# Kernel optimization log

Measured on AMD Instinct MI355X. Metric: run time of the kernel, lower is better.

Reference implementation:

```python
import jax, jax.numpy as jnp
import numpy as np

B = 512       # batch_size
IN = 256      # input_size
H = 512       # hidden_size
OUT = 64      # output_size
N_PAIRS = B - 1   # number of H0 persistence deaths (connected components merges)
TOL = 1e-6    # rtol for torch.isclose
ATOL = 1e-8   # torch default atol
EPS = 0.0     # homology_eps
TARGET_P = 1.0
HOM_P = 1.0
COMP_P = 0.01

_IU = np.triu_indices(B, 1)  # condensed pdist indexing, static


def _mlp(batch, W1, b1, W2, b2, W3, b3, Wout, bout):
    # FeedForward: input->hidden, (n_layers-1) hidden->hidden, hidden->output, ReLU
    h = jax.nn.relu(batch @ W1 + b1)
    h = jax.nn.relu(h @ W2 + b2)
    h = jax.nn.relu(h @ W3 + b3)
    return h @ Wout + bout


def _pdist(y):
    # condensed euclidean pairwise distances, same ordering as torch F.pdist
    d = y[_IU[0]] - y[_IU[1]]                 # [P, OUT]
    return jnp.sqrt(jnp.sum(d * d, axis=-1))  # [P]


def setup_inputs() -> dict:
    key = jax.random.key(0)
    ks = jax.random.split(key, 8)
    batch = jax.random.normal(ks[0], (B, IN), jnp.float32)
    target = jax.random.normal(ks[1], (B, OUT), jnp.float32)
    W1 = jax.random.normal(ks[2], (IN, H), jnp.float32) / np.sqrt(IN)
    W2 = jax.random.normal(ks[3], (H, H), jnp.float32) / np.sqrt(H)
    W3 = jax.random.normal(ks[4], (H, H), jnp.float32) / np.sqrt(H)
    Wout = jax.random.normal(ks[5], (H, OUT), jnp.float32) / np.sqrt(H)
    b1 = jnp.zeros((H,), jnp.float32)
    b2 = jnp.zeros((H,), jnp.float32)
    b3 = jnp.zeros((H,), jnp.float32)
    bout = jnp.zeros((OUT,), jnp.float32)
    # persistence deaths = actual critical pdist values (from the external
    # Vietoris-Rips routine in the original); sample N_PAIRS distinct entries.
    y0 = _mlp(batch, W1, b1, W2, b2, W3, b3, Wout, bout)
    pd0 = np.asarray(_pdist(y0))
    idx = np.random.default_rng(0).choice(pd0.shape[0], N_PAIRS, replace=False)
    persistence_deaths = jnp.asarray(pd0[idx], jnp.float32)
    return {"batch": batch, "target": target,
            "W1": W1, "b1": b1, "W2": W2, "b2": b2, "W3": W3, "b3": b3,
            "Wout": Wout, "bout": bout,
            "persistence_deaths": persistence_deaths}


def reference(batch, target, W1, b1, W2, b2, W3, b3, Wout, bout, persistence_deaths):
    y = _mlp(batch, W1, b1, W2, b2, W3, b3, Wout, bout)   # [B, OUT]
    y_hom = y  # normalize_for_homology = False
    pd = _pdist(y_hom)                                     # [P]
    # vectorized indicator_death over all pairs (replaces per-pair Python loop)
    mask = jnp.any(jnp.isclose(pd[:, None], persistence_deaths[None, :],
                               rtol=TOL, atol=ATOL), axis=1)      # [P] bool
    # homology_dim=0: birth_pdist = 0; norm=1 of selected (death - 0 + eps)
    homology_loss = jnp.sum(jnp.abs(jnp.where(mask, pd + EPS, 0.0)))
    target_loss = jnp.mean((target - y) ** 2)
    compactness_loss = jnp.sum(jnp.abs(y - jnp.mean(y, axis=0, keepdims=True)))
    loss = TARGET_P * target_loss + HOM_P * homology_loss + COMP_P * compactness_loss
    return loss
```

## Files before the change

kernel.cpp:

```cpp
#include <hip/hip_runtime.h>

#define B_    512
#define IN_   256
#define H_    512
#define OUT_  64
#define NDEATH (B_ - 1)
#define NSORT  512
#define RTOL_ 1e-6
#define ATOL_ 1e-8
#define NTHR  512
#define KT    32

typedef __attribute__((ext_vector_type(4))) double d4_t;

__device__ __forceinline__ void lbar() {
    asm volatile("s_waitcnt lgkmcnt(0)" ::: "memory");
    __builtin_amdgcn_s_barrier();
    asm volatile("" ::: "memory");
}

__device__ void sort_windows(const float* __restrict__ deaths,
                             double* sd, double* slo, double* shi, int t) {
    if (t < NSORT) sd[t] = (t < NDEATH) ? (double)deaths[t] : 1e300;
    __syncthreads();
    for (int k = 2; k <= NSORT; k <<= 1) {
        for (int j = k >> 1; j > 0; j >>= 1) {
            if (t < 256) {
                int l = ((t & ~(j - 1)) << 1) | (t & (j - 1));
                int p = l + j;
                bool up = ((l & k) == 0);
                double a = sd[l], b = sd[p];
                if ((a > b) == up) { sd[l] = b; sd[p] = a; }
            }
            __syncthreads();
        }
    }
    if (t < NSORT) {
        double d = sd[t];
        double w = ATOL_ + RTOL_ * fabs(d);
        slo[t] = d - w;
        shi[t] = d + w;
    }
    __syncthreads();
}

template <typename TIN, bool RELU, int N, int K>
__device__ void gemm_dev(const TIN* __restrict__ A, const float* __restrict__ W,
                         const float* __restrict__ bias, double* __restrict__ C,
                         int tile, int t,
                         double (&As)[2][2][KT][33]) {
    const int lane  = t & 63;
    const int wave4 = (t >> 6) & 3;
    const int w2    = t >> 8;
    const int tg    = t & 255;
    const int wm    = wave4 & 1, wn = wave4 >> 1;
    constexpr int nbx = N >> 5;
    const int row0  = (tile / nbx) << 5;
    const int col0  = (tile % nbx) << 5;

    const int akk   = tg & 31;
    const int amm   = tg >> 5;
    const int kbase = w2 * (K >> 1);
    constexpr int nkt = K >> 6;

    const int mrow  = wm * 16 + (lane & 15);
    const int ncol  = wn * 16 + (lane & 15);
    const int kq    = lane >> 4;

    TIN   ar[3][4];
    float br[3][8];

    auto load_a = [&](int rs, int kt) {
        const int k0 = kbase + (kt << 5);
        #pragma unroll
        for (int p = 0; p < 4; ++p)
            ar[rs][p] = A[(size_t)(row0 + amm + 8 * p) * K + k0 + akk];
    };
    auto load_b = [&](int rs, int kt) {
        const int k0 = kbase + (kt << 5);
        const float* wp = W + (size_t)(k0 + kq) * N + col0 + ncol;
        #pragma unroll
        for (int ks = 0; ks < 8; ++ks)
            br[rs][ks] = wp[(size_t)(4 * ks) * N];
    };
    auto stage_a = [&](int rs, int buf) {
        #pragma unroll
        for (int p = 0; p < 4; ++p)
            As[w2][buf][akk][amm + 8 * p] = (double)ar[rs][p];
    };

    load_a(0, 0); load_b(0, 0);
    if (nkt > 1) { load_a(1, 1); load_b(1, 1); }
    if (nkt > 2) { load_a(2, 2); load_b(2, 2); }
    stage_a(0, 0);
    lbar();

    d4_t c4a = {0.0, 0.0, 0.0, 0.0};
    d4_t c4b = {0.0, 0.0, 0.0, 0.0};

    #pragma unroll
    for (int kt = 0; kt < nkt; ++kt) {
        const int cur = kt & 1;
        const int rs  = kt % 3;
        __builtin_amdgcn_s_setprio(1);
        #pragma unroll
        for (int ks = 0; ks < 4; ++ks) {
            double av = As[w2][cur][ks * 4 + kq][mrow];
            c4a = __builtin_amdgcn_mfma_f64_16x16x4f64(av, (double)br[rs][ks],
                                                       c4a, 0, 0, 0);
        }
        #pragma unroll
        for (int ks = 4; ks < 8; ++ks) {
            double av = As[w2][cur][ks * 4 + kq][mrow];
            c4b = __builtin_amdgcn_mfma_f64_16x16x4f64(av, (double)br[rs][ks],
                                                       c4b, 0, 0, 0);
        }
        __builtin_amdgcn_s_setprio(0);
        if (kt + 3 < nkt) { load_a(rs, kt + 3); load_b(rs, kt + 3); }
        if (kt + 1 < nkt) stage_a((kt + 1) % 3, cur ^ 1);
        lbar();
    }

    d4_t c4 = c4a + c4b;

    double (*cEx)[16][17] = (double (*)[16][17])(&As[0][0][0][0]);
    const int r4 = (lane >> 4) * 4;
    if (w2 == 1) {
        #pragma unroll
        for (int r = 0; r < 4; ++r)
            cEx[wave4][r4 + r][lane & 15] = c4[r];
    }
    lbar();
    if (w2 == 0) {
        #pragma unroll
        for (int r = 0; r < 4; ++r) {
            int row = row0 + wm * 16 + r4 + r;
            int col = col0 + wn * 16 + (lane & 15);
            double v = c4[r] + cEx[wave4][r4 + r][lane & 15] + (double)bias[col];
            if (RELU) v = v > 0.0 ? v : 0.0;
            C[(size_t)row * N + col] = v;
        }
    }
}

__device__ __forceinline__ int tile_map(int bid) {
    const int g = (bid & 7) | ((bid >> 7) << 3);
    const int c = (bid >> 3) & 15;
    return g * 16 + c;
}

__global__ __launch_bounds__(NTHR) void g1s_k(
    const float* __restrict__ batch, const float* __restrict__ W1,
    const float* __restrict__ b1, double* __restrict__ hA,
    const float* __restrict__ deaths, double* __restrict__ wbc) {
    __shared__ double As[2][2][KT][33];
    const int t = threadIdx.x, bid = blockIdx.x;
    if (bid == 256) {
        double* sd  = &As[0][0][0][0];
        double* slo = sd + NSORT;
        double* shi = sd + 2 * NSORT;
        sort_windows(deaths, sd, slo, shi, t);
        if (t < NSORT) {
            wbc[t]         = slo[t];
            wbc[NSORT + t] = shi[t];
        }
        return;
    }
    gemm_dev<float, true, H_, IN_>(batch, W1, b1, hA, tile_map(bid), t, As);
}

template <bool RELU>
__global__ __launch_bounds__(NTHR) void gemm_k(
    const double* __restrict__ A, const float* __restrict__ W,
    const float* __restrict__ bias, double* __restrict__ C) {
    __shared__ double As[2][2][KT][33];
    gemm_dev<double, RELU, H_, H_>(A, W, bias, C, tile_map(blockIdx.x),
                                   threadIdx.x, As);
}

__global__ __launch_bounds__(NTHR) void gout_k(
    const double* __restrict__ hC, const float* __restrict__ Wout,
    const float* __restrict__ bout, double* __restrict__ yv) {
    __shared__ double As[2][2][KT][33];
    gemm_dev<double, false, OUT_, H_>(hC, Wout, bout, yv, blockIdx.x,
                                      threadIdx.x, As);
}

__device__ __forceinline__ double pair_val(const double* __restrict__ yrow_s,
                                           const double* __restrict__ yj,
                                           const double* __restrict__ slo,
                                           const double* __restrict__ shi) {
    double s = 0.0;
    #pragma unroll
    for (int d = 0; d < OUT_; d += 2) {
        double2 v = *(const double2*)(yj + d);
        double d0 = yrow_s[d]     - v.x;
        double d1 = yrow_s[d + 1] - v.y;
        s = fma(d0, d0, s);
        s = fma(d1, d1, s);
    }
    double pd = sqrt(s);
    int pos = 0;
    #pragma unroll
    for (int step = NSORT / 2; step; step >>= 1) {
        if (slo[pos + step - 1] <= pd) pos += step;
    }
    bool m = (pos > 0) && (shi[pos - 1] >= pd);
    return m ? pd : 0.0;
}

__device__ void pdist_dev(const double* __restrict__ y,
                          double* __restrict__ hom_part, int bid, int t,
                          double* yA, double* yB,
                          const double* slo, const double* shi) {
    const int iA = bid;
    const int iB = 510 - bid;
    if (t < OUT_)            yA[t]        = y[(size_t)iA * OUT_ + t];
    else if (t < 2 * OUT_)   yB[t - OUT_] = y[(size_t)iB * OUT_ + (t - OUT_)];
    __syncthreads();

    double local = 0.0;
    for (int j = iA + 1 + t; j < B_; j += NTHR)
        local += pair_val(yA, y + (size_t)j * OUT_, slo, shi);
    if (iB != iA)
        for (int j = iB + 1 + t; j < B_; j += NTHR)
            local += pair_val(yB, y + (size_t)j * OUT_, slo, shi);

    for (int off = 32; off; off >>= 1) local += __shfl_down(local, off);
    __shared__ double sw[8];
    int wave = t >> 6, lane = t & 63;
    if (lane == 0) sw[wave] = local;
    __syncthreads();
    if (t == 0) {
        double s = 0.0;
        #pragma unroll
        for (int w = 0; w < 8; ++w) s += sw[w];
        hom_part[bid] = s;
    }
}

__device__ void mc_dev(const float* __restrict__ target,
                       const double* __restrict__ y,
                       double* __restrict__ t_part, double* __restrict__ c_part,
                       int c, int t) {
    const int wave = t >> 6, lane = t & 63;
    double v = y[(size_t)t * OUT_ + c];
    double s = v;
    for (int off = 32; off; off >>= 1) s += __shfl_down(s, off);
    __shared__ double swm[8];
    __shared__ double smean;
    if (lane == 0) swm[wave] = s;
    __syncthreads();
    if (t == 0) {
        double m = 0.0;
        #pragma unroll
        for (int w = 0; w < 8; ++w) m += swm[w];
        smean = m / (double)B_;
    }
    __syncthreads();
    double m = smean;
    double d = (double)target[(size_t)t * OUT_ + c] - v;
    double t_s = d * d;
    double c_s = fabs(v - m);
    for (int off = 32; off; off >>= 1) {
        t_s += __shfl_down(t_s, off);
        c_s += __shfl_down(c_s, off);
    }
    __shared__ double st[8], sc[8];
    if (lane == 0) { st[wave] = t_s; sc[wave] = c_s; }
    __syncthreads();
    if (t == 0) {
        double ts = 0.0, cs = 0.0;
        #pragma unroll
        for (int w = 0; w < 8; ++w) { ts += st[w]; cs += sc[w]; }
        t_part[c] = ts;
        c_part[c] = cs;
    }
}

__global__ __launch_bounds__(NTHR) void pd_k(
    const double* __restrict__ yv, const float* __restrict__ target,
    const double* __restrict__ wbc, double* __restrict__ hom_part,
    double* __restrict__ t_part, double* __restrict__ c_part) {
    __shared__ double slo[NSORT], shi[NSORT];
    __shared__ double yA[OUT_], yB[OUT_];
    const int t = threadIdx.x, bid = blockIdx.x;
    slo[t] = wbc[t];
    shi[t] = wbc[NSORT + t];
    pdist_dev(yv, hom_part, bid, t, yA, yB, slo, shi);
    if (bid < OUT_) mc_dev(target, yv, t_part, c_part, bid, t);
}

__global__ __launch_bounds__(NTHR) void fin_k(
    const double* __restrict__ hom_part, const double* __restrict__ t_part,
    const double* __restrict__ c_part, float* __restrict__ out) {
    const int t = threadIdx.x;
    double h = 0.0, tp = 0.0, cp = 0.0;
    if (t < 256)  h = hom_part[t];
    if (t < OUT_) { tp = t_part[t]; cp = c_part[t]; }
    for (int off = 32; off; off >>= 1) {
        h  += __shfl_down(h,  off);
        tp += __shfl_down(tp, off);
        cp += __shfl_down(cp, off);
    }
    __shared__ double sh[8], stp[8], scp[8];
    int wave = t >> 6, lane = t & 63;
    if (lane == 0) { sh[wave] = h; stp[wave] = tp; scp[wave] = cp; }
    __syncthreads();
    if (t == 0) {
        double hs = 0.0, ts = 0.0, cs = 0.0;
        #pragma unroll
        for (int w = 0; w < 8; ++w) { hs += sh[w]; ts += stp[w]; cs += scp[w]; }
        out[0] = (float)(ts / (double)(B_ * OUT_) + hs + 0.01 * cs);
    }
}

extern "C" void kernel_launch(void* const* d_in, const int* in_sizes, int n_in,
                              void* d_out, int out_size, void* d_ws, size_t ws_size,
                              hipStream_t stream) {
    const float* batch  = (const float*)d_in[0];
    const float* target = (const float*)d_in[1];
    const float* W1     = (const float*)d_in[2];
    const float* b1     = (const float*)d_in[3];
    const float* W2     = (const float*)d_in[4];
    const float* b2     = (const float*)d_in[5];
    const float* W3     = (const float*)d_in[6];
    const float* b3     = (const float*)d_in[7];
    const float* Wout   = (const float*)d_in[8];
    const float* bout   = (const float*)d_in[9];
    const float* deaths = (const float*)d_in[10];
    float* out = (float*)d_out;

    double* hA       = (double*)d_ws;
    double* hB       = hA + (size_t)B_ * H_;
    double* hC       = hB + (size_t)B_ * H_;
    double* yv       = hC + (size_t)B_ * H_;
    double* hom_part = yv + (size_t)B_ * OUT_;
    double* t_part   = hom_part + 256;
    double* c_part   = t_part + OUT_;
    double* wbc      = c_part + OUT_;

    g1s_k<<<dim3(257), dim3(NTHR), 0, stream>>>(batch, W1, b1, hA, deaths, wbc);
    gemm_k<true><<<dim3(256), dim3(NTHR), 0, stream>>>(hA, W2, b2, hB);
    gemm_k<true><<<dim3(256), dim3(NTHR), 0, stream>>>(hB, W3, b3, hC);
    gout_k<<<dim3(32), dim3(NTHR), 0, stream>>>(hC, Wout, bout, yv);
    pd_k<<<dim3(256), dim3(NTHR), 0, stream>>>(yv, target, wbc,
                                               hom_part, t_part, c_part);
    fin_k<<<dim3(1), dim3(NTHR), 0, stream>>>(hom_part, t_part, c_part, out);
}
```

Baseline: 127.9 us.

## Stage whole A k-slab in LDS upfront and drop per-iteration barriers

The GEMM now loads the block's entire A panel for its K half into LDS once before the compute loop, instead of double-buffering 32-wide k-tiles with a barrier every iteration. Only the W operand is still prefetched in registers three iterations ahead. This removes the per-tile LDS barriers and staging in exchange for much larger LDS use: about 135 KB for the K=512 kernels, which may cap occupancy. The kernels also get launch_bounds with a minimum of 2 blocks per CU, which may increase register pressure.

```diff
diff --git a/kernel.cpp b/kernel.cpp
--- a/kernel.cpp
+++ b/kernel.cpp
@@ -9,7 +9,6 @@
 #define RTOL_ 1e-6
 #define ATOL_ 1e-8
 #define NTHR  512
-#define KT    32
 
 typedef __attribute__((ext_vector_type(4))) double d4_t;
 
@@ -47,8 +46,11 @@
 template <typename TIN, bool RELU, int N, int K>
 __device__ void gemm_dev(const TIN* __restrict__ A, const float* __restrict__ W,
                          const float* __restrict__ bias, double* __restrict__ C,
-                         int tile, int t,
-                         double (&As)[2][2][KT][33]) {
+                         int tile, int t, double* __restrict__ lds) {
+    constexpr int nkt = K >> 6;
+    double* AsB = lds;
+    double* cEx = lds + 2 * nkt * 32 * 33;
+
     const int lane  = t & 63;
     const int wave4 = (t >> 6) & 3;
     const int w2    = t >> 8;
@@ -61,21 +63,12 @@
     const int akk   = tg & 31;
     const int amm   = tg >> 5;
     const int kbase = w2 * (K >> 1);
-    constexpr int nkt = K >> 6;
 
     const int mrow  = wm * 16 + (lane & 15);
     const int ncol  = wn * 16 + (lane & 15);
     const int kq    = lane >> 4;
 
-    TIN   ar[3][4];
     float br[3][8];
-
-    auto load_a = [&](int rs, int kt) {
-        const int k0 = kbase + (kt << 5);
-        #pragma unroll
-        for (int p = 0; p < 4; ++p)
-            ar[rs][p] = A[(size_t)(row0 + amm + 8 * p) * K + k0 + akk];
-    };
     auto load_b = [&](int rs, int kt) {
         const int k0 = kbase + (kt << 5);
         const float* wp = W + (size_t)(k0 + kq) * N + col0 + ncol;
@@ -83,16 +76,23 @@
         for (int ks = 0; ks < 8; ++ks)
             br[rs][ks] = wp[(size_t)(4 * ks) * N];
     };
-    auto stage_a = [&](int rs, int buf) {
+    load_b(0, 0);
+    if (nkt > 1) load_b(1, 1);
+    if (nkt > 2) load_b(2, 2);
+
+    TIN tmp[nkt * 4];
+    #pragma unroll
+    for (int q = 0; q < nkt; ++q)
         #pragma unroll
         for (int p = 0; p < 4; ++p)
-            As[w2][buf][akk][amm + 8 * p] = (double)ar[rs][p];
-    };
-
-    load_a(0, 0); load_b(0, 0);
-    if (nkt > 1) { load_a(1, 1); load_b(1, 1); }
-    if (nkt > 2) { load_a(2, 2); load_b(2, 2); }
-    stage_a(0, 0);
+            tmp[q * 4 + p] =
+                A[(size_t)(row0 + amm + 8 * p) * K + kbase + (q << 5) + akk];
+    #pragma unroll
+    for (int q = 0; q < nkt; ++q)
+        #pragma unroll
+        for (int p = 0; p < 4; ++p)
+            AsB[((w2 * nkt + q) * 32 + akk) * 33 + amm + 8 * p] =
+                (double)tmp[q * 4 + p];
     lbar();
 
     d4_t c4a = {0.0, 0.0, 0.0, 0.0};
@@ -100,35 +100,32 @@
 
     #pragma unroll
     for (int kt = 0; kt < nkt; ++kt) {
-        const int cur = kt & 1;
-        const int rs  = kt % 3;
+        const int rs = kt % 3;
+        const double* ap = &AsB[(size_t)((w2 * nkt + kt) * 32) * 33];
         __builtin_amdgcn_s_setprio(1);
         #pragma unroll
         for (int ks = 0; ks < 4; ++ks) {
-            double av = As[w2][cur][ks * 4 + kq][mrow];
+            double av = ap[(ks * 4 + kq) * 33 + mrow];
             c4a = __builtin_amdgcn_mfma_f64_16x16x4f64(av, (double)br[rs][ks],
                                                        c4a, 0, 0, 0);
         }
         #pragma unroll
         for (int ks = 4; ks < 8; ++ks) {
-            double av = As[w2][cur][ks * 4 + kq][mrow];
+            double av = ap[(ks * 4 + kq) * 33 + mrow];
             c4b = __builtin_amdgcn_mfma_f64_16x16x4f64(av, (double)br[rs][ks],
                                                        c4b, 0, 0, 0);
         }
         __builtin_amdgcn_s_setprio(0);
-        if (kt + 3 < nkt) { load_a(rs, kt + 3); load_b(rs, kt + 3); }
-        if (kt + 1 < nkt) stage_a((kt + 1) % 3, cur ^ 1);
-        lbar();
+        if (kt + 3 < nkt) load_b(rs, kt + 3);
     }
 
     d4_t c4 = c4a + c4b;
 
-    double (*cEx)[16][17] = (double (*)[16][17])(&As[0][0][0][0]);
     const int r4 = (lane >> 4) * 4;
     if (w2 == 1) {
         #pragma unroll
         for (int r = 0; r < 4; ++r)
-            cEx[wave4][r4 + r][lane & 15] = c4[r];
+            cEx[(wave4 * 16 + r4 + r) * 17 + (lane & 15)] = c4[r];
     }
     lbar();
     if (w2 == 0) {
@@ -136,7 +133,8 @@
         for (int r = 0; r < 4; ++r) {
             int row = row0 + wm * 16 + r4 + r;
             int col = col0 + wn * 16 + (lane & 15);
-            double v = c4[r] + cEx[wave4][r4 + r][lane & 15] + (double)bias[col];
+            double v = c4[r] + cEx[(wave4 * 16 + r4 + r) * 17 + (lane & 15)]
+                     + (double)bias[col];
             if (RELU) v = v > 0.0 ? v : 0.0;
             C[(size_t)row * N + col] = v;
         }
@@ -149,16 +147,16 @@
     return g * 16 + c;
 }
 
-__global__ __launch_bounds__(NTHR) void g1s_k(
+__global__ __launch_bounds__(NTHR, 2) void g1s_k(
     const float* __restrict__ batch, const float* __restrict__ W1,
     const float* __restrict__ b1, double* __restrict__ hA,
     const float* __restrict__ deaths, double* __restrict__ wbc) {
-    __shared__ double As[2][2][KT][33];
+    __shared__ double lds[2 * 4 * 32 * 33 + 4 * 16 * 17];
     const int t = threadIdx.x, bid = blockIdx.x;
     if (bid == 256) {
-        double* sd  = &As[0][0][0][0];
-        double* slo = sd + NSORT;
-        double* shi = sd + 2 * NSORT;
+        double* sd  = lds;
+        double* slo = lds + NSORT;
+        double* shi = lds + 2 * NSORT;
         sort_windows(deaths, sd, slo, shi, t);
         if (t < NSORT) {
             wbc[t]         = slo[t];
@@ -166,24 +164,24 @@
         }
         return;
     }
-    gemm_dev<float, true, H_, IN_>(batch, W1, b1, hA, tile_map(bid), t, As);
+    gemm_dev<float, true, H_, IN_>(batch, W1, b1, hA, tile_map(bid), t, lds);
 }
 
 template <bool RELU>
-__global__ __launch_bounds__(NTHR) void gemm_k(
+__global__ __launch_bounds__(NTHR, 2) void gemm_k(
     const double* __restrict__ A, const float* __restrict__ W,
     const float* __restrict__ bias, double* __restrict__ C) {
-    __shared__ double As[2][2][KT][33];
+    __shared__ double lds[2 * 8 * 32 * 33 + 4 * 16 * 17];
     gemm_dev<double, RELU, H_, H_>(A, W, bias, C, tile_map(blockIdx.x),
-                                   threadIdx.x, As);
-}
-
-__global__ __launch_bounds__(NTHR) void gout_k(
+                                   threadIdx.x, lds);
+}
+
+__global__ __launch_bounds__(NTHR, 2) void gout_k(
     const double* __restrict__ hC, const float* __restrict__ Wout,
     const float* __restrict__ bout, double* __restrict__ yv) {
-    __shared__ double As[2][2][KT][33];
+    __shared__ double lds[2 * 8 * 32 * 33 + 4 * 16 * 17];
     gemm_dev<double, false, OUT_, H_>(hC, Wout, bout, yv, blockIdx.x,
-                                      threadIdx.x, As);
+                                      threadIdx.x, lds);
 }
 
 __device__ __forceinline__ double pair_val(const double* __restrict__ yrow_s,
```

Result: no change. 129.8 us (+1.5%).
